# Kernel tuning notes

Hardware: AMD Instinct MI355X
Metric: run time of the kernel (lower is better)

## Reference

```python
import jax, jax.numpy as jnp
import numpy as np
from jax import lax

SEQ, BSZ = 64, 32
NTOK, NINP, NHID, NLAYERS = 50000, 512, 1024, 2
BN_EPS = 1e-5


def setup_inputs() -> dict:
    key = jax.random.key(0)
    ks = jax.random.split(key, 12)
    s = 0.05
    return {
        "input_ids": jax.random.randint(ks[0], (SEQ, BSZ), 0, NTOK),
        "hx": jnp.zeros((NLAYERS, BSZ, NHID), jnp.float32),
        "cx": jnp.zeros((NLAYERS, BSZ, NHID), jnp.float32),
        "emb_w": jax.random.normal(ks[1], (NTOK, NINP), jnp.float32) * 0.01,
        "Wih0": jax.random.normal(ks[2], (4 * NHID, NINP), jnp.float32) * s,
        "Whh0": jax.random.normal(ks[3], (4 * NHID, NHID), jnp.float32) * s,
        "bih0": jnp.zeros((4 * NHID,), jnp.float32),
        "bhh0": jnp.zeros((4 * NHID,), jnp.float32),
        "Wih1": jax.random.normal(ks[4], (4 * NHID, NHID), jnp.float32) * s,
        "Whh1": jax.random.normal(ks[5], (4 * NHID, NHID), jnp.float32) * s,
        "bih1": jnp.zeros((4 * NHID,), jnp.float32),
        "bhh1": jnp.zeros((4 * NHID,), jnp.float32),
        "Wp": jax.random.normal(ks[6], (NINP, NHID), jnp.float32) * s,
        "bp": jnp.zeros((NINP,), jnp.float32),
        "Wd": jax.random.normal(ks[7], (NTOK, NINP), jnp.float32) * 0.01,
        "bd": jnp.zeros((NTOK,), jnp.float32),
    }


def _lstm_cell(x, h, c, Wih, Whh, bih, bhh):
    # torch.nn.LSTMCell math; gates packed as [i, f, g, o]
    gates = x @ Wih.T + bih + h @ Whh.T + bhh  # [B, 4H]
    i, f, g, o = jnp.split(gates, 4, axis=-1)
    i = jax.nn.sigmoid(i)
    f = jax.nn.sigmoid(f)
    g = jnp.tanh(g)
    o = jax.nn.sigmoid(o)
    c2 = f * c + i * g
    h2 = o * jnp.tanh(c2)
    return h2, c2


def reference(input_ids, hx, cx, emb_w, Wih0, Whh0, bih0, bhh0,
              Wih1, Whh1, bih1, bhh1, Wp, bp, Wd, bd):
    # eval mode: drop / internal_drop / rdrop are identity; rmask == 1
    emb = emb_w[input_ids]  # [S, B, ninp]
    layers = ((Wih0, Whh0, bih0, bhh0), (Wih1, Whh1, bih1, bhh1))

    def step(carry, x_t):
        h, c = carry  # each [nlayers, B, H]
        hi = x_t
        hs, cs = [], []
        for j in range(NLAYERS):
            Wih, Whh, bih, bhh = layers[j]
            hj, cj = _lstm_cell(hi, h[j], c[j], Wih, Whh, bih, bhh)
            hs.append(hj)
            cs.append(cj)
            hi = hj
        return (jnp.stack(hs, 0), jnp.stack(cs, 0)), hi

    (hxf, cxf), out = lax.scan(step, (hx, cx), emb)  # out: [S, B, H]
    flat = out.reshape(-1, NHID)  # [S*B, H]
    # predictor: Linear -> BatchNorm1d (eval: running_mean=0, running_var=1,
    # gamma=1, beta=0) -> Tanh
    pre = flat @ Wp.T + bp
    p = jnp.tanh(pre * (1.0 / jnp.sqrt(jnp.float32(1.0 + BN_EPS))))
    decoded = p @ Wd.T + bd  # [S*B, ntoken]
    return decoded.reshape(SEQ, BSZ, NTOK), (hxf, cxf)
```

## Files before the change

kernel.cpp:

```cpp
#include <hip/hip_runtime.h>
#include <hip/hip_bf16.h>

using bf16 = __hip_bfloat16;
typedef __attribute__((ext_vector_type(8))) short short8;
typedef __attribute__((ext_vector_type(4))) float f32x4;

#define MFMA_BF16(A,B,C) __builtin_amdgcn_mfma_f32_16x16x32_bf16((A),(B),(C),0,0,0)

static __device__ __forceinline__ unsigned bf16bits(float f) {
  union { bf16 h; unsigned short u; } cv; cv.h = __float2bfloat16(f); return cv.u;
}

static __device__ __forceinline__ void gload16(const void* g, void* l) {
  __builtin_amdgcn_global_load_lds(
      (const __attribute__((address_space(1))) void*)g,
      (__attribute__((address_space(3))) void*)l, 16, 0, 0);
}

template<int EPI>
__global__ __launch_bounds__(256)
void gemm_bt(const bf16* __restrict__ A, const bf16* __restrict__ B,
             const float* __restrict__ bias1, const float* __restrict__ bias2,
             float* __restrict__ Cf, bf16* __restrict__ Cb,
             int M, int N, int K, int Nreal)
{
  __shared__ __align__(1024) bf16 As[128*32];
  __shared__ __align__(1024) bf16 Bs[128*32];
  const int tid  = threadIdx.x;
  const int wave = tid >> 6, lane = tid & 63;
  const int wr = wave >> 1, wc = wave & 1;
  const int row0 = blockIdx.y * 128;
  const int col0 = blockIdx.x * 128;

  f32x4 acc[4][4];
  #pragma unroll
  for (int m = 0; m < 4; ++m)
    #pragma unroll
    for (int n = 0; n < 4; ++n) { f32x4 z = {0.f,0.f,0.f,0.f}; acc[m][n] = z; }

  const int r_sub = lane >> 2;
  const int kc    = lane & 3;

  for (int k0 = 0; k0 < K; k0 += 32) {
    __syncthreads();
    #pragma unroll
    for (int j = 0; j < 2; ++j) {
      const int rb = wave*32 + j*16;
      gload16(A + (size_t)(row0 + rb + r_sub)*K + k0 + kc*8,
              (void*)((char*)As + (size_t)rb*64));
      gload16(B + (size_t)(col0 + rb + r_sub)*K + k0 + kc*8,
              (void*)((char*)Bs + (size_t)rb*64));
    }
    __syncthreads();

    short8 af[4], bfv[4];
    #pragma unroll
    for (int m = 0; m < 4; ++m)
      af[m] = *(const short8*)(As + (wr*64 + m*16 + (lane&15))*32 + (lane>>4)*8);
    #pragma unroll
    for (int n = 0; n < 4; ++n)
      bfv[n] = *(const short8*)(Bs + (wc*64 + n*16 + (lane&15))*32 + (lane>>4)*8);
    #pragma unroll
    for (int m = 0; m < 4; ++m)
      #pragma unroll
      for (int n = 0; n < 4; ++n)
        acc[m][n] = MFMA_BF16(af[m], bfv[n], acc[m][n]);
  }

  const float BN_SCALE = 0.9999950000374997f;
  #pragma unroll
  for (int m = 0; m < 4; ++m) {
    const int rg0 = row0 + wr*64 + m*16 + ((lane>>4)<<2);
    #pragma unroll
    for (int n = 0; n < 4; ++n) {
      const int cg = col0 + wc*64 + n*16 + (lane&15);
      if (EPI == 2) {
        const int bq = cg >> 4, q = cg & 15;
        const int orig = (q>>2)*1024 + bq*4 + (q&3);
        const float bb = bias1[orig] + bias2[orig];
        #pragma unroll
        for (int j = 0; j < 4; ++j) {
          const int row = rg0 + j;
          Cf[((size_t)bq*64 + (row>>5))*512 + (size_t)(row&31)*16 + q]
              = acc[m][n][j] + bb;
        }
      } else if (cg < Nreal) {
        float bb = 0.f;
        if (bias1) bb += bias1[cg];
        if (bias2) bb += bias2[cg];
        #pragma unroll
        for (int j = 0; j < 4; ++j) {
          float v = acc[m][n][j] + bb;
          v = tanhf(v * BN_SCALE);
          Cb[(size_t)(rg0+j)*Nreal + cg] = __float2bfloat16(v);
        }
      }
    }
  }
}

__global__ __launch_bounds__(512, 2)
void gemm_dec(const bf16* __restrict__ A, const bf16* __restrict__ B,
              const float* __restrict__ bias, float* __restrict__ C,
              int M, int N, int K, int Nreal)
{
  __shared__ __align__(1024) bf16 As[256*32];
  __shared__ __align__(1024) bf16 Bs[256*32];
  const int tid  = threadIdx.x;
  const int wave = tid >> 6, lane = tid & 63;
  const int wr = wave >> 2, wc = wave & 3;
  const int row0 = blockIdx.y * 256;
  const int col0 = blockIdx.x * 256;

  f32x4 acc[8][4];
  #pragma unroll
  for (int m = 0; m < 8; ++m)
    #pragma unroll
    for (int n = 0; n < 4; ++n) { f32x4 z = {0.f,0.f,0.f,0.f}; acc[m][n] = z; }

  const int r_sub = lane >> 2;
  const int kc    = lane & 3;

  for (int k0 = 0; k0 < K; k0 += 32) {
    __syncthreads();
    #pragma unroll
    for (int j = 0; j < 2; ++j) {
      const int rb = wave*32 + j*16;
      gload16(A + (size_t)(row0 + rb + r_sub)*K + k0 + kc*8,
              (void*)((char*)As + (size_t)rb*64));
      gload16(B + (size_t)(col0 + rb + r_sub)*K + k0 + kc*8,
              (void*)((char*)Bs + (size_t)rb*64));
    }
    __syncthreads();

    short8 af[8], bfv[4];
    #pragma unroll
    for (int m = 0; m < 8; ++m)
      af[m] = *(const short8*)(As + (wr*128 + m*16 + (lane&15))*32 + (lane>>4)*8);
    #pragma unroll
    for (int n = 0; n < 4; ++n)
      bfv[n] = *(const short8*)(Bs + (wc*64 + n*16 + (lane&15))*32 + (lane>>4)*8);
    #pragma unroll
    for (int m = 0; m < 8; ++m)
      #pragma unroll
      for (int n = 0; n < 4; ++n)
        acc[m][n] = MFMA_BF16(af[m], bfv[n], acc[m][n]);
  }

  #pragma unroll
  for (int m = 0; m < 8; ++m) {
    const int rg0 = row0 + wr*128 + m*16 + ((lane>>4)<<2);
    #pragma unroll
    for (int n = 0; n < 4; ++n) {
      const int cg = col0 + wc*64 + n*16 + (lane&15);
      if (cg < Nreal) {
        const float bb = bias[cg];
        #pragma unroll
        for (int j = 0; j < 4; ++j)
          C[(size_t)(rg0+j)*Nreal + cg] = acc[m][n][j] + bb;
      }
    }
  }
}

__global__ __launch_bounds__(256, 1)
void k_lstm_persist(const bf16* __restrict__ hinit, const float* __restrict__ cx,
                    const bf16* __restrict__ Wpack, const float* __restrict__ g0p,
                    const float* __restrict__ bih1, const float* __restrict__ bhh1,
                    bf16* __restrict__ h0_all, bf16* __restrict__ h1_all,
                    float* __restrict__ tail, unsigned* __restrict__ flags)
{
  const int b    = blockIdx.x;
  const int tid  = threadIdx.x;
  const int wave = tid >> 6, lane = tid & 63;

  __shared__ __align__(1024) bf16 Wlds[96*512];
  __shared__ float P[4][2][32][20];

  const bf16* wbase = Wpack + (size_t)b * 96 * 512;
  #pragma unroll
  for (int it = 0; it < 24; ++it) {
    const int chunk = it*4 + wave;
    gload16(wbase + (size_t)chunk*512 + lane*8,
            (void*)((char*)Wlds + (size_t)chunk*1024));
  }

  const int layer = tid >> 7;
  const int cell  = tid & 127;
  const int r     = cell >> 2;
  const int hc    = cell & 3;
  const int col   = b*4 + hc;
  float creg = cx[(size_t)layer*32768 + (size_t)r*1024 + col];
  float bsum[4];
  #pragma unroll
  for (int g = 0; g < 4; ++g)
    bsum[g] = (layer == 1) ? (bih1[g*1024 + col] + bhh1[g*1024 + col]) : 0.f;

  const int arow = lane & 15;
  const int koff = (lane >> 4) * 8;

  const unsigned* fp0 = flags + (lane*4+0)*32;
  const unsigned* fp1 = flags + (lane*4+1)*32;
  const unsigned* fp2 = flags + (lane*4+2)*32;
  const unsigned* fp3 = flags + (lane*4+3)*32;

  __syncthreads();

  for (int s = 0; s < 65; ++s) {
    const bf16* hA = (s == 0) ? hinit           : h0_all + (size_t)(s-1)*32768;
    const bf16* hB = (s <= 1) ? (hinit + 32768) : h1_all + (size_t)(s-2)*32768;

    short8 a0[8], a1[8], c0[8], c1[8];
    #pragma unroll
    for (int i = 0; i < 8; ++i) {
      const int kb = wave*256 + i*32 + koff;
      a0[i] = *(const short8*)(hA + (size_t)arow*1024      + kb);
      a1[i] = *(const short8*)(hA + (size_t)(arow+16)*1024 + kb);
      c0[i] = *(const short8*)(hB + (size_t)arow*1024      + kb);
      c1[i] = *(const short8*)(hB + (size_t)(arow+16)*1024 + kb);
    }
    float gpre[4] = {0.f, 0.f, 0.f, 0.f};
    if (layer == 0 && s < 64) {
      const float* gr = g0p + ((size_t)(b*64 + s)*32 + r)*16;
      #pragma unroll
      for (int g = 0; g < 4; ++g) gpre[g] = gr[g*4 + hc];
    }

    f32x4 z = {0.f,0.f,0.f,0.f};
    f32x4 acc00 = z, acc01 = z, acc10 = z, acc11 = z;
    #pragma unroll
    for (int i = 0; i < 8; ++i) {
      const int ks = wave*8 + i;
      short8 w0 = *(const short8*)(Wlds + ((size_t)(     ks)*64 + lane)*8);
      short8 w1 = *(const short8*)(Wlds + ((size_t)(32 + ks)*64 + lane)*8);
      short8 w2 = *(const short8*)(Wlds + ((size_t)(64 + ks)*64 + lane)*8);
      acc00 = MFMA_BF16(a0[i], w0, acc00);
      acc01 = MFMA_BF16(a1[i], w0, acc01);
      acc10 = MFMA_BF16(a0[i], w1, acc10);
      acc11 = MFMA_BF16(a1[i], w1, acc11);
      acc10 = MFMA_BF16(c0[i], w2, acc10);
      acc11 = MFMA_BF16(c1[i], w2, acc11);
    }

    #pragma unroll
    for (int j = 0; j < 4; ++j) {
      const int pr = (lane >> 4)*4 + j;
      P[wave][0][pr     ][lane & 15] = acc00[j];
      P[wave][0][pr + 16][lane & 15] = acc01[j];
      P[wave][1][pr     ][lane & 15] = acc10[j];
      P[wave][1][pr + 16][lane & 15] = acc11[j];
    }
    __syncthreads();

    const int t = s - layer;
    if (t >= 0 && t < 64) {
      float v[4];
      #pragma unroll
      for (int g = 0; g < 4; ++g) {
        const int j = g*4 + hc;
        v[g] = P[0][layer][r][j] + P[1][layer][r][j]
             + P[2][layer][r][j] + P[3][layer][r][j] + bsum[g] + gpre[g];
      }
      const float iv = 1.f/(1.f + expf(-v[0]));
      const float fv = 1.f/(1.f + expf(-v[1]));
      const float gv = tanhf(v[2]);
      const float ov = 1.f/(1.f + expf(-v[3]));
      creg = fv*creg + iv*gv;
      const float hn = ov*tanhf(creg);
      unsigned hu  = bf16bits(hn);
      unsigned p01 = hu | ((unsigned)__shfl_xor((int)hu, 1) << 16);
      unsigned p23 = (unsigned)__shfl_xor((int)p01, 2);
      if (hc == 0) {
        bf16* hp = (layer ? h1_all : h0_all) + (size_t)t*32768 + (size_t)r*1024 + b*4;
        unsigned long long v64 = (unsigned long long)p01
                               | ((unsigned long long)p23 << 32);
        __hip_atomic_store((unsigned long long*)hp, v64,
                           __ATOMIC_RELAXED, __HIP_MEMORY_SCOPE_AGENT);
      }
      if (t == 63) {
        tail[(size_t)layer*32768 + (size_t)r*1024 + col]         = hn;
        tail[65536 + (size_t)layer*32768 + (size_t)r*1024 + col] = creg;
      }
    }
    if (s == 64) break;

    __syncthreads();
    if (tid == 0) {
      asm volatile("global_store_dword %0, %1, off sc0 sc1\n\t"
                   "s_waitcnt vmcnt(0)"
                   :: "v"(flags + b*32), "v"((unsigned)(s + 1)) : "memory");
    }
    if (wave == 0) {
      const unsigned su = (unsigned)s;
      for (;;) {
        unsigned v0, v1, v2, v3;
        asm volatile("global_load_dword %0, %1, off sc0 sc1" : "=v"(v0) : "v"(fp0));
        asm volatile("global_load_dword %0, %1, off sc0 sc1" : "=v"(v1) : "v"(fp1));
        asm volatile("global_load_dword %0, %1, off sc0 sc1" : "=v"(v2) : "v"(fp2));
        asm volatile("global_load_dword %0, %1, off sc0 sc1" : "=v"(v3) : "v"(fp3));
        asm volatile("s_waitcnt vmcnt(0)" ::: "memory");
        bool ok = (v0 > su) & (v1 > su) & (v2 > su) & (v3 > su);
        if (__all(ok)) break;
        __builtin_amdgcn_s_sleep(1);
      }
    }
    __syncthreads();
    asm volatile("" ::: "memory");
    __builtin_amdgcn_sched_barrier(0);
  }
}

__global__ __launch_bounds__(256)
void k_pack(const float* __restrict__ Whh0, const float* __restrict__ Wih1,
            const float* __restrict__ Whh1, bf16* __restrict__ Wpack)
{
  const int b = blockIdx.x;
  #pragma unroll 4
  for (int it = 0; it < 24; ++it) {
    const int idx = it*256 + threadIdx.x;
    const int chunkp = idx >> 6;
    const int l = idx & 63;
    const int p = chunkp >> 5, c = chunkp & 31;
    const float* W = (p == 0) ? Whh0 : (p == 1 ? Wih1 : Whh1);
    const int j = l & 15;
    const int row = (j>>2)*1024 + b*4 + (j&3);
    const int k = c*32 + (l>>4)*8;
    const float* src = W + (size_t)row*1024 + k;
    bf16* dst = Wpack + ((size_t)(b*96 + chunkp)*64 + l)*8;
    #pragma unroll
    for (int q = 0; q < 8; ++q) dst[q] = __float2bfloat16(src[q]);
  }
}

__global__ void k_cvt(const float* __restrict__ s, bf16* __restrict__ d, long n) {
  long i = (long)blockIdx.x*blockDim.x + threadIdx.x;
  if (i < n) d[i] = __float2bfloat16(s[i]);
}

__global__ void k_cvt_perm(const float* __restrict__ src, bf16* __restrict__ dst) {
  const int n = blockIdx.x;
  const int orig = ((n>>2)&3)*1024 + (n>>4)*4 + (n&3);
  const float4 v = ((const float4*)(src + (size_t)orig*512))[threadIdx.x];
  bf16* d = dst + (size_t)n*512 + threadIdx.x*4;
  d[0] = __float2bfloat16(v.x); d[1] = __float2bfloat16(v.y);
  d[2] = __float2bfloat16(v.z); d[3] = __float2bfloat16(v.w);
}

__global__ void k_cvt_pad(const float* __restrict__ s, bf16* __restrict__ d,
                          long n, long nrows_real, int rowlen) {
  long i = (long)blockIdx.x*blockDim.x + threadIdx.x;
  if (i < n) {
    long r = i / rowlen;
    d[i] = (r < nrows_real) ? __float2bfloat16(s[i]) : __float2bfloat16(0.f);
  }
}

__global__ void k_init(const float* __restrict__ hx, bf16* __restrict__ hinit,
                       unsigned* __restrict__ flags) {
  int i = blockIdx.x*blockDim.x + threadIdx.x;
  if (i < 8192) flags[i] = 0u;
  if (i < 65536) hinit[i] = __float2bfloat16(hx[i]);
}

__global__ void k_embed(const int* __restrict__ ids, const float* __restrict__ emb_w,
                        bf16* __restrict__ out) {
  const int row = blockIdx.x;
  const int tok = ids[row];
  const float4 v = ((const float4*)(emb_w + (size_t)tok*512))[threadIdx.x];
  bf16* d = out + (size_t)row*512 + threadIdx.x*4;
  d[0] = __float2bfloat16(v.x); d[1] = __float2bfloat16(v.y);
  d[2] = __float2bfloat16(v.z); d[3] = __float2bfloat16(v.w);
}

extern "C" void kernel_launch(void* const* d_in, const int* in_sizes, int n_in,
                              void* d_out, int out_size, void* d_ws, size_t ws_size,
                              hipStream_t stream) {
  const int*   ids  = (const int*)d_in[0];
  const float* hx   = (const float*)d_in[1];
  const float* cx   = (const float*)d_in[2];
  const float* embw = (const float*)d_in[3];
  const float* Wih0 = (const float*)d_in[4];
  const float* Whh0 = (const float*)d_in[5];
  const float* bih0 = (const float*)d_in[6];
  const float* bhh0 = (const float*)d_in[7];
  const float* Wih1 = (const float*)d_in[8];
  const float* Whh1 = (const float*)d_in[9];
  const float* bih1 = (const float*)d_in[10];
  const float* bhh1 = (const float*)d_in[11];
  const float* Wp   = (const float*)d_in[12];
  const float* bp   = (const float*)d_in[13];
  const float* Wd   = (const float*)d_in[14];
  const float* bd   = (const float*)d_in[15];
  float* out = (float*)d_out;

  char* w = (char*)d_ws;
  bf16* Wih0b = (bf16*)w; w += 4096l*512*2;
  bf16* Wpack = (bf16*)w; w += 256l*96*64*8*2;
  bf16* Wpb   = (bf16*)w; w += 512l*1024*2;
  bf16* Wdb   = (bf16*)w; w += 50176l*512*2;
  bf16* embb  = (bf16*)w; w += 2048l*512*2;
  float* g0p  = (float*)w; w += 2048l*4096*4;
  bf16* h0a   = (bf16*)w; w += 2048l*1024*2;
  bf16* h1a   = (bf16*)w; w += 2048l*1024*2;
  bf16* hinit = (bf16*)w; w += 2l*32*1024*2;
  bf16* pb    = (bf16*)w; w += 2048l*512*2;
  unsigned* flags = (unsigned*)w; w += 8192*4;

  k_cvt_perm<<<4096, 128, 0, stream>>>(Wih0, Wih0b);
  k_cvt<<<(512l*1024 + 255)/256, 256, 0, stream>>>(Wp, Wpb, 512l*1024);
  k_cvt_pad<<<(50176l*512 + 255)/256, 256, 0, stream>>>(Wd, Wdb, 50176l*512, 50000, 512);
  k_init<<<256, 256, 0, stream>>>(hx, hinit, flags);
  k_embed<<<2048, 128, 0, stream>>>(ids, embw, embb);
  k_pack<<<256, 256, 0, stream>>>(Whh0, Wih1, Whh1, Wpack);

  gemm_bt<2><<<dim3(32, 16), 256, 0, stream>>>(
      embb, Wih0b, bih0, bhh0, g0p, nullptr, 2048, 4096, 512, 4096);

  float* tail = out + 102400000l;
  k_lstm_persist<<<256, 256, 0, stream>>>(hinit, cx, Wpack, g0p, bih1, bhh1,
                                          h0a, h1a, tail, flags);

  gemm_bt<1><<<dim3(4, 16), 256, 0, stream>>>(
      h1a, Wpb, bp, nullptr, nullptr, pb, 2048, 512, 1024, 512);

  gemm_dec<<<dim3(196, 8), 512, 0, stream>>>(
      pb, Wdb, bd, out, 2048, 50176, 512, 50000);
}
```

Measured before the change: 731.8 us.

## Double-buffer LDS tiles in decoder GEMM to overlap global loads with MFMA

Turns the decoder GEMM's single LDS buffer into two, prefetching the next K tile with global_load_lds while MFMAs run on the current one. Explicit vmcnt waits and barriers replace the two syncthreads per iteration. The aim is to hide global memory latency in the large 50000-column projection. In exchange LDS use per block doubles to 64KB, which may cut occupancy from the declared 2 blocks per CU, and the hand-written waitcnt counts must match the number of loads issued per stage.

```diff
diff --git a/kernel.cpp b/kernel.cpp
--- a/kernel.cpp
+++ b/kernel.cpp
@@ -104,8 +104,8 @@
               const float* __restrict__ bias, float* __restrict__ C,
               int M, int N, int K, int Nreal)
 {
-  __shared__ __align__(1024) bf16 As[256*32];
-  __shared__ __align__(1024) bf16 Bs[256*32];
+  __shared__ __align__(1024) bf16 As[2*256*32];
+  __shared__ __align__(1024) bf16 Bs[2*256*32];
   const int tid  = threadIdx.x;
   const int wave = tid >> 6, lane = tid & 63;
   const int wr = wave >> 2, wc = wave & 3;
@@ -121,30 +121,47 @@
   const int r_sub = lane >> 2;
   const int kc    = lane & 3;
 
-  for (int k0 = 0; k0 < K; k0 += 32) {
-    __syncthreads();
+  auto STAGE = [&](int sl, int k0) {
     #pragma unroll
     for (int j = 0; j < 2; ++j) {
       const int rb = wave*32 + j*16;
       gload16(A + (size_t)(row0 + rb + r_sub)*K + k0 + kc*8,
-              (void*)((char*)As + (size_t)rb*64));
+              (void*)((char*)As + (size_t)sl*16384 + (size_t)rb*64));
       gload16(B + (size_t)(col0 + rb + r_sub)*K + k0 + kc*8,
-              (void*)((char*)Bs + (size_t)rb*64));
-    }
-    __syncthreads();
-
+              (void*)((char*)Bs + (size_t)sl*16384 + (size_t)rb*64));
+    }
+  };
+
+  const int NT = K >> 5;
+  STAGE(0, 0);
+  if (NT > 1) STAGE(1, 32);
+
+  for (int kk = 0; kk < NT; ++kk) {
+    const int cur = kk & 1;
+    if (kk == NT - 1) asm volatile("s_waitcnt vmcnt(0)" ::: "memory");
+    else              asm volatile("s_waitcnt vmcnt(4)" ::: "memory");
+    __builtin_amdgcn_sched_barrier(0);
+    __builtin_amdgcn_s_barrier();
+
+    const bf16* Ab = As + (size_t)cur*8192;
+    const bf16* Bb = Bs + (size_t)cur*8192;
     short8 af[8], bfv[4];
     #pragma unroll
     for (int m = 0; m < 8; ++m)
-      af[m] = *(const short8*)(As + (wr*128 + m*16 + (lane&15))*32 + (lane>>4)*8);
+      af[m] = *(const short8*)(Ab + (wr*128 + m*16 + (lane&15))*32 + (lane>>4)*8);
     #pragma unroll
     for (int n = 0; n < 4; ++n)
-      bfv[n] = *(const short8*)(Bs + (wc*64 + n*16 + (lane&15))*32 + (lane>>4)*8);
+      bfv[n] = *(const short8*)(Bb + (wc*64 + n*16 + (lane&15))*32 + (lane>>4)*8);
     #pragma unroll
     for (int m = 0; m < 8; ++m)
       #pragma unroll
       for (int n = 0; n < 4; ++n)
         acc[m][n] = MFMA_BF16(af[m], bfv[n], acc[m][n]);
+
+    asm volatile("s_waitcnt lgkmcnt(0)" ::: "memory");
+    __builtin_amdgcn_sched_barrier(0);
+    __builtin_amdgcn_s_barrier();
+    if (kk + 2 < NT) STAGE(cur, (kk + 2) * 32);
   }
 
   #pragma unroll
```

Measured after the change: 723.4 us. About the same (-1.2%).
